# Kernel tuning notes

Hardware: AMD Instinct MI355X
Metric: run time of the kernel (lower is better)

The kernel has to match this reference:

```python
import jax, jax.numpy as jnp
import numpy as np

DIM, HEADS, MLP_HID = 1024, 16, 4096
B, N = 2, 2048
EPS = 1e-5

def setup_inputs() -> dict:
    key = jax.random.key(0)
    ks = jax.random.split(key, 8)
    s = lambda fan_in: 1.0 / np.sqrt(fan_in)
    return {
        "x": jax.random.normal(ks[0], (B, N, DIM), jnp.float32),
        "ln1_w": jnp.ones((DIM,), jnp.float32),
        "ln1_b": jnp.zeros((DIM,), jnp.float32),
        # weights stored [in, out] (transpose of torch Linear.weight)
        "qkv_w": jax.random.normal(ks[1], (DIM, 3 * DIM), jnp.float32) * s(DIM),
        "proj_w": jax.random.normal(ks[2], (DIM, DIM), jnp.float32) * s(DIM),
        "proj_b": jnp.zeros((DIM,), jnp.float32),
        "ln2_w": jnp.ones((DIM,), jnp.float32),
        "ln2_b": jnp.zeros((DIM,), jnp.float32),
        "fc1_w": jax.random.normal(ks[3], (DIM, MLP_HID), jnp.float32) * s(DIM),
        "fc1_b": jnp.zeros((MLP_HID,), jnp.float32),
        "fc2_w": jax.random.normal(ks[4], (MLP_HID, DIM), jnp.float32) * s(MLP_HID),
        "fc2_b": jnp.zeros((DIM,), jnp.float32),
    }

def _layernorm(x, w, b):
    mu = jnp.mean(x, axis=-1, keepdims=True)
    var = jnp.mean(jnp.square(x - mu), axis=-1, keepdims=True)
    return (x - mu) * jax.lax.rsqrt(var + EPS) * w + b

def reference(x, ln1_w, ln1_b, qkv_w, proj_w, proj_b, ln2_w, ln2_b, fc1_w, fc1_b, fc2_w, fc2_b):
    Bn, Nn, C = x.shape
    H, D = HEADS, C // HEADS
    scale = D ** -0.5

    # --- attention sub-block (pre-norm, residual) ---
    h = _layernorm(x, ln1_w, ln1_b)
    qkv = (h @ qkv_w).reshape(Bn, Nn, 3, H, D)
    q, k, v = jnp.moveaxis(qkv, 2, 0)  # each [B, N, H, D]
    attn = jnp.einsum('bnhd,bmhd->bhnm', q, k) * scale
    attn = jax.nn.softmax(attn, axis=-1)
    o = jnp.einsum('bhnm,bmhd->bnhd', attn, v).reshape(Bn, Nn, C)
    x = x + (o @ proj_w + proj_b)

    # --- MLP sub-block (pre-norm, residual) ---
    h = _layernorm(x, ln2_w, ln2_b)
    h = jax.nn.gelu(h @ fc1_w + fc1_b, approximate=False)
    x = x + (h @ fc2_w + fc2_b)
    return x
```

## Files before the change

### kernel.cpp

```cpp
#include <hip/hip_runtime.h>
#include <hip/hip_bf16.h>

typedef __attribute__((ext_vector_type(4))) float  f32x4;
typedef __attribute__((ext_vector_type(8))) short  short8;
typedef __attribute__((ext_vector_type(8))) unsigned short ushort8;
typedef __attribute__((ext_vector_type(4))) unsigned short u16x4;
typedef unsigned short u16;

__device__ __forceinline__ u16 f2bf(float f) {
    unsigned int u = __builtin_bit_cast(unsigned int, f);
    return (u16)((u + 0x7fffu + ((u >> 16) & 1u)) >> 16);
}

__device__ __forceinline__ unsigned cvtpk(float lo, float hi) {
    unsigned r;
    asm("v_cvt_pk_bf16_f32 %0, %1, %2" : "=v"(r) : "v"(lo), "v"(hi));
    return r;
}

__device__ __forceinline__ f32x4 mfma16(short8 a, short8 b, f32x4 c) {
    return __builtin_amdgcn_mfma_f32_16x16x32_bf16(a, b, c, 0, 0, 0);
}

__device__ __forceinline__ float fexp2(float x) {
    float r;
    asm("v_exp_f32 %0, %1" : "=v"(r) : "v"(x));
    return r;
}

__device__ __forceinline__ float fgelu(float v) {
    const float t = v * v;
    const float u = v * (-2.302118f - 0.102944f * t);
    return v / (1.0f + fexp2(u));
}

__device__ __forceinline__ void gload_lds16(const u16* g, u16* l) {
    __builtin_amdgcn_global_load_lds(
        (__attribute__((address_space(1))) void*)(uintptr_t)(g),
        (__attribute__((address_space(3))) void*)(unsigned)(uintptr_t)(l),
        16, 0, 0);
}

__device__ __forceinline__ void BAR() {
    __builtin_amdgcn_sched_barrier(0);
    __builtin_amdgcn_s_barrier();
    __builtin_amdgcn_sched_barrier(0);
}

__global__ __launch_bounds__(256) void tcast_kernel(const float* __restrict__ W,
                                                    u16* __restrict__ Wt,
                                                    int K, int N) {
    __shared__ float tile[32][33];
    const int tx = threadIdx.x & 31, ty = threadIdx.x >> 5;
    const int c0 = blockIdx.x * 32;
    const int r0 = blockIdx.y * 32;
#pragma unroll
    for (int i = 0; i < 32; i += 8)
        tile[ty + i][tx] = W[(size_t)(r0 + ty + i) * N + c0 + tx];
    __syncthreads();
#pragma unroll
    for (int i = 0; i < 32; i += 8)
        Wt[(size_t)(c0 + ty + i) * K + r0 + tx] = f2bf(tile[tx][ty + i]);
}

__global__ __launch_bounds__(256) void ln_kernel(const float* __restrict__ x,
                                                 const float* __restrict__ w,
                                                 const float* __restrict__ b,
                                                 u16* __restrict__ out) {
    const int row = blockIdx.x;
    const int tid = threadIdx.x;
    const float4 v = ((const float4*)(x + (size_t)row * 1024))[tid];
    float s1 = v.x + v.y + v.z + v.w;
    float s2 = v.x * v.x + v.y * v.y + v.z * v.z + v.w * v.w;
#pragma unroll
    for (int m = 1; m < 64; m <<= 1) { s1 += __shfl_xor(s1, m); s2 += __shfl_xor(s2, m); }
    __shared__ float red1[4], red2[4];
    const int wave = tid >> 6, lane = tid & 63;
    if (lane == 0) { red1[wave] = s1; red2[wave] = s2; }
    __syncthreads();
    s1 = red1[0] + red1[1] + red1[2] + red1[3];
    s2 = red2[0] + red2[1] + red2[2] + red2[3];
    const float mean = s1 * (1.0f / 1024.0f);
    const float var  = s2 * (1.0f / 1024.0f) - mean * mean;
    const float rstd = rsqrtf(var + 1e-5f);
    const float4 wv = ((const float4*)w)[tid];
    const float4 bv = ((const float4*)b)[tid];
    u16x4 o;
    o[0] = f2bf((v.x - mean) * rstd * wv.x + bv.x);
    o[1] = f2bf((v.y - mean) * rstd * wv.y + bv.y);
    o[2] = f2bf((v.z - mean) * rstd * wv.z + bv.z);
    o[3] = f2bf((v.w - mean) * rstd * wv.w + bv.w);
    *(u16x4*)(out + (size_t)row * 1024 + tid * 4) = o;
}

template <int BN, int HAS_BIAS, int HAS_RES, int DO_GELU, int OUT_BF16>
__global__ __launch_bounds__(512, 2) void gemm8_kernel(const u16* __restrict__ A,
                                                       const u16* __restrict__ Bt,
                                                       const float* __restrict__ bias,
                                                       const float* __restrict__ res,
                                                       void* __restrict__ Cout,
                                                       int M, int N, int K) {
    constexpr int NTN = BN / 64;
    constexpr int BH  = BN / 2;
    constexpr int BSW = BH / 64;
    __shared__ __align__(16) u16 Asl[2][2][128 * 64];
    __shared__ __align__(16) u16 Bsl[2][2][BH * 64];
    const int tid = threadIdx.x;
    const int wave = tid >> 6, lane = tid & 63;
    const int wr = wave >> 2, wc = wave & 3;
    const int fq = lane >> 4, fr = lane & 15;
    const size_t bm = (size_t)blockIdx.y * 256, bn = (size_t)blockIdx.x * BN;
    const int hb = wc >> 1;
    const int brow0 = (wc & 1) * (BN / 4);

    const int rx = fr & 7;
    const int ko0 = ((0 + fq) ^ rx) * 8;
    const int ko1 = ((4 + fq) ^ rx) * 8;

    f32x4 acc[8][NTN] = {};

    auto STAGE = [&](int buf, int k0) {
#pragma unroll
        for (int h = 0; h < 2; h++)
#pragma unroll
            for (int s = 0; s < 2; s++) {
                const int task = tid + s * 512;
                const int row = task >> 3, seg2 = (task & 7) ^ (row & 7);
                gload_lds16(A + (bm + h * 128 + row) * (size_t)K + k0 + seg2 * 8,
                            &Asl[buf][h][(wave * 64 + s * 512) * 8]);
            }
#pragma unroll
        for (int h = 0; h < 2; h++)
#pragma unroll
            for (int s = 0; s < BSW; s++) {
                const int task = tid + s * 512;
                const int row = task >> 3, seg2 = (task & 7) ^ (row & 7);
                gload_lds16(Bt + (bn + h * BH + row) * (size_t)K + k0 + seg2 * 8,
                            &Bsl[buf][h][(wave * 64 + s * 512) * 8]);
            }
    };

    STAGE(0, 0);
    asm volatile("s_waitcnt vmcnt(0)" ::: "memory");
    __builtin_amdgcn_s_barrier();
    int cur = 0;

    for (int k0 = 0; k0 < K; k0 += 64) {
        short8 bfr[NTN][2];
#pragma unroll
        for (int q = 0; q < 4; q++) {
            if (q == 0) {
#pragma unroll
                for (int nt = 0; nt < NTN; nt++) {
                    const int r16 = brow0 + nt * 16 + fr;
                    bfr[nt][0] = *(const short8*)&Bsl[cur][hb][r16 * 64 + ko0];
                    bfr[nt][1] = *(const short8*)&Bsl[cur][hb][r16 * 64 + ko1];
                }
            }
            short8 afr[2][2];
#pragma unroll
            for (int m2 = 0; m2 < 2; m2++) {
                const int r16 = (q * 2 + m2) * 16 + fr;
                afr[m2][0] = *(const short8*)&Asl[cur][wr][r16 * 64 + ko0];
                afr[m2][1] = *(const short8*)&Asl[cur][wr][r16 * 64 + ko1];
            }
            if (q == 0 && k0 + 64 < K) STAGE(cur ^ 1, k0 + 64);
            BAR();
            __builtin_amdgcn_s_setprio(1);
#pragma unroll
            for (int ksu = 0; ksu < 2; ksu++)
#pragma unroll
                for (int m2 = 0; m2 < 2; m2++)
#pragma unroll
                    for (int nt = 0; nt < NTN; nt++)
                        acc[q * 2 + m2][nt] = mfma16(afr[m2][ksu], bfr[nt][ksu],
                                                     acc[q * 2 + m2][nt]);
            __builtin_amdgcn_s_setprio(0);
            if (q == 3) {
                asm volatile("s_waitcnt vmcnt(0)" ::: "memory");
            }
            BAR();
        }
        cur ^= 1;
    }
#pragma unroll
    for (int mt = 0; mt < 8; mt++) {
#pragma unroll
        for (int nt = 0; nt < NTN; nt++) {
            const size_t col = bn + wc * (BN / 4) + nt * 16 + fr;
            const float bb = HAS_BIAS ? bias[col] : 0.0f;
#pragma unroll
            for (int j = 0; j < 4; j++) {
                const size_t row = bm + wr * 128 + mt * 16 + fq * 4 + j;
                float v = acc[mt][nt][j] + bb;
                if (DO_GELU) v = fgelu(v);
                if (HAS_RES) v += res[row * N + col];
                if (OUT_BF16) ((u16*)Cout)[row * N + col] = f2bf(v);
                else          ((float*)Cout)[row * N + col] = v;
            }
        }
    }
}

template <int HAS_BIAS, int HAS_RES, int DO_GELU, int OUT_BF16>
__global__ __launch_bounds__(256) void gemm_kernel(const u16* __restrict__ A,
                                                   const u16* __restrict__ Bt,
                                                   const float* __restrict__ bias,
                                                   const float* __restrict__ res,
                                                   void* __restrict__ Cout,
                                                   int M, int N, int K) {
    __shared__ __align__(16) u16 As[2][128 * 64];
    __shared__ __align__(16) u16 Bs[2][128 * 64];
    const int tid = threadIdx.x;
    const int wave = tid >> 6, lane = tid & 63;
    const int wr = wave >> 1, wc = wave & 1;
    const int fq = lane >> 4, fr = lane & 15;
    const size_t bm = (size_t)blockIdx.y * 128, bn = (size_t)blockIdx.x * 128;
    const int lr = lane >> 3, seg = lane & 7;
    const int seg2 = seg ^ (lr & 7);

    const u16* Ab = A  + bm * (size_t)K + seg2 * 8;
    const u16* Bb = Bt + bn * (size_t)K + seg2 * 8;

    const int rx = fr & 7;
    const int ko0 = ((0 + fq) ^ rx) * 8;
    const int ko1 = ((4 + fq) ^ rx) * 8;

    f32x4 acc[4][4] = {};

    auto STAGE = [&](int buf, int k0) {
#pragma unroll
        for (int i = 0; i < 4; i++) {
            const int r = wave * 32 + i * 8 + lr;
            gload_lds16(Ab + (size_t)r * K + k0, &As[buf][(wave * 4 + i) * 512]);
            gload_lds16(Bb + (size_t)r * K + k0, &Bs[buf][(wave * 4 + i) * 512]);
        }
    };

    STAGE(0, 0);
    __syncthreads();
    int cur = 0;

    for (int k0 = 0; k0 < K; k0 += 64) {
        if (k0 + 64 < K) STAGE(cur ^ 1, k0 + 64);
#pragma unroll
        for (int ks = 0; ks < 2; ks++) {
            const int ko = ks ? ko1 : ko0;
            short8 af[4], bf[4];
#pragma unroll
            for (int t = 0; t < 4; t++) {
                af[t] = *(const short8*)&As[cur][(wr * 64 + t * 16 + fr) * 64 + ko];
                bf[t] = *(const short8*)&Bs[cur][(wc * 64 + t * 16 + fr) * 64 + ko];
            }
#pragma unroll
            for (int mt = 0; mt < 4; mt++)
#pragma unroll
                for (int nt = 0; nt < 4; nt++)
                    acc[mt][nt] = mfma16(af[mt], bf[nt], acc[mt][nt]);
        }
        __syncthreads();
        cur ^= 1;
    }
#pragma unroll
    for (int mt = 0; mt < 4; mt++) {
#pragma unroll
        for (int nt = 0; nt < 4; nt++) {
            const size_t col = bn + wc * 64 + nt * 16 + fr;
            const float bb = HAS_BIAS ? bias[col] : 0.0f;
#pragma unroll
            for (int j = 0; j < 4; j++) {
                const size_t row = bm + wr * 64 + mt * 16 + fq * 4 + j;
                float v = acc[mt][nt][j] + bb;
                if (DO_GELU) v = fgelu(v);
                if (HAS_RES) v += res[row * N + col];
                if (OUT_BF16) ((u16*)Cout)[row * N + col] = f2bf(v);
                else          ((float*)Cout)[row * N + col] = v;
            }
        }
    }
}

__global__ __launch_bounds__(512) void attn_kernel(const u16* __restrict__ qkv,
                                                   u16* __restrict__ O) {
    const int bh = blockIdx.x;
    const int b = bh >> 4, h = bh & 15;
    const int qb = blockIdx.y;
    const int tid = threadIdx.x, wave = tid >> 6, lane = tid & 63;
    const int fq = lane >> 4, fr = lane & 15;
    __shared__ __align__(16) u16 Ks[2][64 * 64];
    __shared__ __align__(16) u16 Vt[2][64 * 64];
    __shared__ __align__(16) u16 Pl[8][16 * 64];

    const size_t base = (size_t)b * 2048 * 3072;
    const int q0 = qb * 128 + wave * 16;

    short8 qf[2];
#pragma unroll
    for (int ks = 0; ks < 2; ks++)
        qf[ks] = *(const short8*)(qkv + base + (size_t)(q0 + fr) * 3072 + h * 64 + ks * 32 + fq * 8);

    const u16* kp = qkv + base + 1024 + (size_t)h * 64;
    const u16* vp = qkv + base + 2048 + (size_t)h * 64;
    const int krow = tid >> 3, kseg = tid & 7;
    const int kpos = (kseg ^ (krow & 7)) * 8;
    const int vkey = tid & 63, vdc = tid >> 6;

    const int rx = fr & 7;
    const int ko0 = ((0 + fq) ^ rx) * 8;
    const int ko1 = ((4 + fq) ^ rx) * 8;

    f32x4 accO[4] = {};
    float mq = -1e30f, lq = 0.0f;

    const float c = 0.125f * 1.44269504f;
    const float THR = 11.5f;

    ushort8 kreg = *(const ushort8*)(kp + (size_t)krow * 3072 + kseg * 8);
    ushort8 vreg = *(const ushort8*)(vp + (size_t)vkey * 3072 + vdc * 8);
    *(ushort8*)&Ks[0][krow * 64 + kpos] = kreg;
#pragma unroll
    for (int j = 0; j < 8; j++) {
        const int row = vdc * 8 + j;
        Vt[0][row * 64 + ((vkey >> 3) ^ (row & 7)) * 8 + (vkey & 7)] = vreg[j];
    }
    __syncthreads();
    int cur = 0;

    for (int kt = 0; kt < 32; kt++) {
        if (kt < 31) {
            kreg = *(const ushort8*)(kp + (size_t)((kt + 1) * 64 + krow) * 3072 + kseg * 8);
            vreg = *(const ushort8*)(vp + (size_t)((kt + 1) * 64 + vkey) * 3072 + vdc * 8);
        }
        f32x4 s[4];
#pragma unroll
        for (int nt = 0; nt < 4; nt++) {
            f32x4 a = {};
            short8 kf0 = *(const short8*)&Ks[cur][(nt * 16 + fr) * 64 + ko0];
            short8 kf1 = *(const short8*)&Ks[cur][(nt * 16 + fr) * 64 + ko1];
            a = mfma16(kf0, qf[0], a);
            a = mfma16(kf1, qf[1], a);
            s[nt] = a;
        }
        float pm = fmaxf(fmaxf(s[0][0], s[0][1]), fmaxf(s[0][2], s[0][3]));
#pragma unroll
        for (int nt = 1; nt < 4; nt++) {
            const float m01 = fmaxf(s[nt][0], s[nt][1]);
            const float m23 = fmaxf(s[nt][2], s[nt][3]);
            pm = fmaxf(pm, fmaxf(m01, m23));
        }
        pm = fmaxf(pm, __shfl_xor(pm, 16));
        pm = fmaxf(pm, __shfl_xor(pm, 32));
        const float pms = pm * c;
        float aq = 1.0f;
        if (!__all(pms <= mq + THR)) {
            const float mn = fmaxf(mq, pms);
            aq = fexp2(mq - mn);
            mq = mn;
            float ar[4];
#pragma unroll
            for (int j = 0; j < 4; j++) ar[j] = __shfl(aq, fq * 4 + j);
#pragma unroll
            for (int dt = 0; dt < 4; dt++)
#pragma unroll
                for (int j = 0; j < 4; j++) accO[dt][j] *= ar[j];
        }
        float lsum = 0.0f;
#pragma unroll
        for (int nt = 0; nt < 4; nt++)
#pragma unroll
            for (int j = 0; j < 4; j++) {
                const float pij = fexp2(__builtin_fmaf(s[nt][j], c, -mq));
                s[nt][j] = pij;
                lsum += pij;
            }
        lsum += __shfl_xor(lsum, 16);
        lsum += __shfl_xor(lsum, 32);
        lq = lq * aq + lsum;
#pragma unroll
        for (int nt = 0; nt < 4; nt++) {
            uint2 pw;
            pw.x = cvtpk(s[nt][0], s[nt][1]);
            pw.y = cvtpk(s[nt][2], s[nt][3]);
            const int chunk = nt * 2 + (fq >> 1);
            *(uint2*)&Pl[wave][fr * 64 + (chunk ^ rx) * 8 + (fq & 1) * 4] = pw;
        }
#pragma unroll
        for (int ks = 0; ks < 2; ks++) {
            const int ko = ks ? ko1 : ko0;
            short8 pf = *(const short8*)&Pl[wave][fr * 64 + ko];
#pragma unroll
            for (int dt = 0; dt < 4; dt++) {
                short8 vf = *(const short8*)&Vt[cur][(dt * 16 + fr) * 64 + ko];
                accO[dt] = mfma16(pf, vf, accO[dt]);
            }
        }
        if (kt < 31) {
            *(ushort8*)&Ks[cur ^ 1][krow * 64 + kpos] = kreg;
#pragma unroll
            for (int j = 0; j < 8; j++) {
                const int row = vdc * 8 + j;
                Vt[cur ^ 1][row * 64 + ((vkey >> 3) ^ (row & 7)) * 8 + (vkey & 7)] = vreg[j];
            }
        }
        __syncthreads();
        cur ^= 1;
    }
    float rq[4];
#pragma unroll
    for (int j = 0; j < 4; j++) rq[j] = 1.0f / __shfl(lq, fq * 4 + j);
#pragma unroll
    for (int dt = 0; dt < 4; dt++)
#pragma unroll
        for (int j = 0; j < 4; j++) {
            const float v = accO[dt][j] * rq[j];
            O[(size_t)(b * 2048 + q0 + fq * 4 + j) * 1024 + h * 64 + dt * 16 + fr] = f2bf(v);
        }
}

extern "C" void kernel_launch(void* const* d_in, const int* in_sizes, int n_in,
                              void* d_out, int out_size, void* d_ws, size_t ws_size,
                              hipStream_t stream) {
    (void)in_sizes; (void)n_in; (void)out_size; (void)ws_size;
    const float* x     = (const float*)d_in[0];
    const float* ln1w  = (const float*)d_in[1];
    const float* ln1b  = (const float*)d_in[2];
    const float* qkvw  = (const float*)d_in[3];
    const float* projw = (const float*)d_in[4];
    const float* projb = (const float*)d_in[5];
    const float* ln2w  = (const float*)d_in[6];
    const float* ln2b  = (const float*)d_in[7];
    const float* fc1w  = (const float*)d_in[8];
    const float* fc1b  = (const float*)d_in[9];
    const float* fc2w  = (const float*)d_in[10];
    const float* fc2b  = (const float*)d_in[11];

    char* p = (char*)d_ws;
    auto alloc = [&](size_t bytes) { void* r = p; p += (bytes + 255) & ~(size_t)255; return r; };
    u16* wt_qkv  = (u16*)alloc(3072ull * 1024 * 2);
    u16* wt_proj = (u16*)alloc(1024ull * 1024 * 2);
    u16* wt_fc1  = (u16*)alloc(4096ull * 1024 * 2);
    u16* wt_fc2  = (u16*)alloc(1024ull * 4096 * 2);
    u16* h1      = (u16*)alloc(4096ull * 1024 * 2);
    u16* qkv     = (u16*)alloc(4096ull * 3072 * 2);
    u16* attn_o  = (u16*)alloc(4096ull * 1024 * 2);
    u16* h2      = (u16*)alloc(4096ull * 1024 * 2);
    u16* mlp_h   = (u16*)alloc(4096ull * 4096 * 2);
    float* x1 = (float*)d_out;

    tcast_kernel<<<dim3(96, 32),  256, 0, stream>>>(qkvw,  wt_qkv, 1024, 3072);
    tcast_kernel<<<dim3(32, 32),  256, 0, stream>>>(projw, wt_proj, 1024, 1024);
    tcast_kernel<<<dim3(128, 32), 256, 0, stream>>>(fc1w,  wt_fc1, 1024, 4096);
    tcast_kernel<<<dim3(32, 128), 256, 0, stream>>>(fc2w,  wt_fc2, 4096, 1024);

    ln_kernel<<<4096, 256, 0, stream>>>(x, ln1w, ln1b, h1);
    gemm8_kernel<256, 0, 0, 0, 1><<<dim3(12, 16), 512, 0, stream>>>(h1, wt_qkv, nullptr, nullptr, qkv, 4096, 3072, 1024);
    attn_kernel<<<dim3(32, 16), 512, 0, stream>>>(qkv, attn_o);
    gemm_kernel<1, 1, 0, 0><<<dim3(8, 32), 256, 0, stream>>>(attn_o, wt_proj, projb, x, x1, 4096, 1024, 1024);

    ln_kernel<<<4096, 256, 0, stream>>>(x1, ln2w, ln2b, h2);
    gemm8_kernel<256, 1, 0, 1, 1><<<dim3(16, 16), 512, 0, stream>>>(h2, wt_fc1, fc1b, nullptr, mlp_h, 4096, 4096, 1024);
    gemm_kernel<1, 1, 0, 0><<<dim3(8, 32), 256, 0, stream>>>(mlp_h, wt_fc2, fc2b, x1, d_out, 4096, 1024, 4096);
}
```

Before: 235.6 us.

## Restructure gemm8 into 4-slot K=32 pipeline with three stages in flight

Replaces the double-buffered K=64 staging in the 256x256 GEMM with a 4-slot ring of K=32 chunks, prefetching three chunks ahead and waiting on partial vmcnt instead of draining fully each iteration. The LDS swizzle and fragment loads are reworked for 32-wide rows, and each iteration splits into two MFMA halves separated by barriers. The aim is to hide global-load latency better in the QKV and FC1 GEMMs. In exchange there are more barriers per unit of K, and the BN template parameter is removed.

```diff
diff --git a/kernel.cpp b/kernel.cpp
--- a/kernel.cpp
+++ b/kernel.cpp
@@ -93,101 +93,85 @@
     *(u16x4*)(out + (size_t)row * 1024 + tid * 4) = o;
 }
 
-template <int BN, int HAS_BIAS, int HAS_RES, int DO_GELU, int OUT_BF16>
+template <int HAS_BIAS, int HAS_RES, int DO_GELU, int OUT_BF16>
 __global__ __launch_bounds__(512, 2) void gemm8_kernel(const u16* __restrict__ A,
                                                        const u16* __restrict__ Bt,
                                                        const float* __restrict__ bias,
                                                        const float* __restrict__ res,
                                                        void* __restrict__ Cout,
                                                        int M, int N, int K) {
-    constexpr int NTN = BN / 64;
-    constexpr int BH  = BN / 2;
-    constexpr int BSW = BH / 64;
-    __shared__ __align__(16) u16 Asl[2][2][128 * 64];
-    __shared__ __align__(16) u16 Bsl[2][2][BH * 64];
+    __shared__ __align__(16) u16 Ag[4][256 * 32];
+    __shared__ __align__(16) u16 Bg[4][256 * 32];
     const int tid = threadIdx.x;
     const int wave = tid >> 6, lane = tid & 63;
     const int wr = wave >> 2, wc = wave & 3;
     const int fq = lane >> 4, fr = lane & 15;
-    const size_t bm = (size_t)blockIdx.y * 256, bn = (size_t)blockIdx.x * BN;
-    const int hb = wc >> 1;
-    const int brow0 = (wc & 1) * (BN / 4);
-
-    const int rx = fr & 7;
-    const int ko0 = ((0 + fq) ^ rx) * 8;
-    const int ko1 = ((4 + fq) ^ rx) * 8;
-
-    f32x4 acc[8][NTN] = {};
-
-    auto STAGE = [&](int buf, int k0) {
-#pragma unroll
-        for (int h = 0; h < 2; h++)
-#pragma unroll
-            for (int s = 0; s < 2; s++) {
-                const int task = tid + s * 512;
-                const int row = task >> 3, seg2 = (task & 7) ^ (row & 7);
-                gload_lds16(A + (bm + h * 128 + row) * (size_t)K + k0 + seg2 * 8,
-                            &Asl[buf][h][(wave * 64 + s * 512) * 8]);
-            }
-#pragma unroll
-        for (int h = 0; h < 2; h++)
-#pragma unroll
-            for (int s = 0; s < BSW; s++) {
-                const int task = tid + s * 512;
-                const int row = task >> 3, seg2 = (task & 7) ^ (row & 7);
-                gload_lds16(Bt + (bn + h * BH + row) * (size_t)K + k0 + seg2 * 8,
-                            &Bsl[buf][h][(wave * 64 + s * 512) * 8]);
-            }
+    const size_t bm = (size_t)blockIdx.y * 256, bn = (size_t)blockIdx.x * 256;
+
+    const int ko = (fq ^ ((fr >> 1) & 3)) * 8;
+
+    const int srow = tid >> 2;
+    const int scol = ((tid & 3) ^ ((tid >> 3) & 3)) * 8;
+    const u16* Asrc = A  + (bm + srow) * (size_t)K + scol;
+    const u16* Bsrc = Bt + (bn + srow) * (size_t)K + scol;
+    const int sdst = wave * 512;
+
+    f32x4 acc[8][4] = {};
+
+    auto STAGE_G = [&](int slot, int kc) {
+#pragma unroll
+        for (int s = 0; s < 2; s++) {
+            gload_lds16(Asrc + (size_t)s * 128 * K + kc, &Ag[slot][sdst + s * 4096]);
+            gload_lds16(Bsrc + (size_t)s * 128 * K + kc, &Bg[slot][sdst + s * 4096]);
+        }
     };
 
-    STAGE(0, 0);
-    asm volatile("s_waitcnt vmcnt(0)" ::: "memory");
+    const int NG = K >> 5;
+    STAGE_G(0, 0); STAGE_G(1, 32); STAGE_G(2, 64);
+    __builtin_amdgcn_sched_barrier(0);
+    asm volatile("s_waitcnt vmcnt(8)" ::: "memory");
     __builtin_amdgcn_s_barrier();
-    int cur = 0;
-
-    for (int k0 = 0; k0 < K; k0 += 64) {
-        short8 bfr[NTN][2];
-#pragma unroll
-        for (int q = 0; q < 4; q++) {
-            if (q == 0) {
-#pragma unroll
-                for (int nt = 0; nt < NTN; nt++) {
-                    const int r16 = brow0 + nt * 16 + fr;
-                    bfr[nt][0] = *(const short8*)&Bsl[cur][hb][r16 * 64 + ko0];
-                    bfr[nt][1] = *(const short8*)&Bsl[cur][hb][r16 * 64 + ko1];
-                }
-            }
-            short8 afr[2][2];
-#pragma unroll
-            for (int m2 = 0; m2 < 2; m2++) {
-                const int r16 = (q * 2 + m2) * 16 + fr;
-                afr[m2][0] = *(const short8*)&Asl[cur][wr][r16 * 64 + ko0];
-                afr[m2][1] = *(const short8*)&Asl[cur][wr][r16 * 64 + ko1];
-            }
-            if (q == 0 && k0 + 64 < K) STAGE(cur ^ 1, k0 + 64);
-            BAR();
-            __builtin_amdgcn_s_setprio(1);
-#pragma unroll
-            for (int ksu = 0; ksu < 2; ksu++)
-#pragma unroll
-                for (int m2 = 0; m2 < 2; m2++)
-#pragma unroll
-                    for (int nt = 0; nt < NTN; nt++)
-                        acc[q * 2 + m2][nt] = mfma16(afr[m2][ksu], bfr[nt][ksu],
-                                                     acc[q * 2 + m2][nt]);
-            __builtin_amdgcn_s_setprio(0);
-            if (q == 3) {
-                asm volatile("s_waitcnt vmcnt(0)" ::: "memory");
-            }
-            BAR();
-        }
-        cur ^= 1;
+
+    for (int g = 0; g < NG; g++) {
+        const int slot = g & 3;
+        short8 bfr[4], af[4];
+#pragma unroll
+        for (int nt = 0; nt < 4; nt++)
+            bfr[nt] = *(const short8*)&Bg[slot][(wc * 64 + nt * 16 + fr) * 32 + ko];
+#pragma unroll
+        for (int m2 = 0; m2 < 4; m2++)
+            af[m2] = *(const short8*)&Ag[slot][(wr * 128 + m2 * 16 + fr) * 32 + ko];
+        if (g + 3 < NG) STAGE_G((g + 3) & 3, (g + 3) * 32);
+        BAR();
+        __builtin_amdgcn_s_setprio(1);
+#pragma unroll
+        for (int m2 = 0; m2 < 4; m2++)
+#pragma unroll
+            for (int nt = 0; nt < 4; nt++)
+                acc[m2][nt] = mfma16(af[m2], bfr[nt], acc[m2][nt]);
+        __builtin_amdgcn_s_setprio(0);
+        BAR();
+#pragma unroll
+        for (int m2 = 0; m2 < 4; m2++)
+            af[m2] = *(const short8*)&Ag[slot][(wr * 128 + (m2 + 4) * 16 + fr) * 32 + ko];
+        BAR();
+        __builtin_amdgcn_s_setprio(1);
+#pragma unroll
+        for (int m2 = 0; m2 < 4; m2++)
+#pragma unroll
+            for (int nt = 0; nt < 4; nt++)
+                acc[m2 + 4][nt] = mfma16(af[m2], bfr[nt], acc[m2 + 4][nt]);
+        __builtin_amdgcn_s_setprio(0);
+        __builtin_amdgcn_sched_barrier(0);
+        if (g < NG - 3) { asm volatile("s_waitcnt vmcnt(8)" ::: "memory"); }
+        else            { asm volatile("s_waitcnt vmcnt(0)" ::: "memory"); }
+        BAR();
     }
 #pragma unroll
     for (int mt = 0; mt < 8; mt++) {
 #pragma unroll
-        for (int nt = 0; nt < NTN; nt++) {
-            const size_t col = bn + wc * (BN / 4) + nt * 16 + fr;
+        for (int nt = 0; nt < 4; nt++) {
+            const size_t col = bn + wc * 64 + nt * 16 + fr;
             const float bb = HAS_BIAS ? bias[col] : 0.0f;
 #pragma unroll
             for (int j = 0; j < 4; j++) {
@@ -453,11 +437,11 @@
     tcast_kernel<<<dim3(32, 128), 256, 0, stream>>>(fc2w,  wt_fc2, 4096, 1024);
 
     ln_kernel<<<4096, 256, 0, stream>>>(x, ln1w, ln1b, h1);
-    gemm8_kernel<256, 0, 0, 0, 1><<<dim3(12, 16), 512, 0, stream>>>(h1, wt_qkv, nullptr, nullptr, qkv, 4096, 3072, 1024);
+    gemm8_kernel<0, 0, 0, 1><<<dim3(12, 16), 512, 0, stream>>>(h1, wt_qkv, nullptr, nullptr, qkv, 4096, 3072, 1024);
     attn_kernel<<<dim3(32, 16), 512, 0, stream>>>(qkv, attn_o);
     gemm_kernel<1, 1, 0, 0><<<dim3(8, 32), 256, 0, stream>>>(attn_o, wt_proj, projb, x, x1, 4096, 1024, 1024);
 
     ln_kernel<<<4096, 256, 0, stream>>>(x1, ln2w, ln2b, h2);
-    gemm8_kernel<256, 1, 0, 1, 1><<<dim3(16, 16), 512, 0, stream>>>(h2, wt_fc1, fc1b, nullptr, mlp_h, 4096, 4096, 1024);
+    gemm8_kernel<1, 0, 1, 1><<<dim3(16, 16), 512, 0, stream>>>(h2, wt_fc1, fc1b, nullptr, mlp_h, 4096, 4096, 1024);
     gemm_kernel<1, 1, 0, 0><<<dim3(8, 32), 256, 0, stream>>>(mlp_h, wt_fc2, fc2b, x1, d_out, 4096, 1024, 4096);
 }
```

Result: no change. 235.9 us (+0.1%).
